# Kernel tuning notes

Hardware: AMD Instinct MI355X
Metric: run time of the kernel (lower is better)

## Reference

```python
import jax, jax.numpy as jnp
import numpy as np

VOL_RANGE = (-40.0, -40.0, -1.0, 40.0, 40.0, 5.4)
VOXEL = 0.8
SCENE = tuple(int((VOL_RANGE[i + 3] - VOL_RANGE[i]) / VOXEL) for i in range(3))  # (100, 100, 8)
B, G, F = 1, 128, 16


def _make_grid():
    # generate_grid(scene_shape, offset=0.5) * voxel_size + vol_range[:3]
    axes = [(jnp.arange(s, dtype=jnp.float32) + 0.5) * VOXEL + VOL_RANGE[i]
            for i, s in enumerate(SCENE)]
    gx, gy, gz = jnp.meshgrid(*axes, indexing='ij')
    return jnp.stack([gx, gy, gz], axis=-1).reshape(-1, 3)  # (N, 3)


def setup_inputs() -> dict:
    key = jax.random.key(0)
    k1, k2, k3, k4 = jax.random.split(key, 4)
    lo = jnp.array(VOL_RANGE[:3], dtype=jnp.float32)
    hi = jnp.array(VOL_RANGE[3:], dtype=jnp.float32)
    means3d = lo + jax.random.uniform(k1, (B, G, 3), dtype=jnp.float32) * (hi - lo)
    opacities = jax.random.uniform(k2, (B, G, 1), dtype=jnp.float32)
    features = jax.random.normal(k3, (B, G, F), dtype=jnp.float32)
    A = jax.random.normal(k4, (B, G, 3, 3), dtype=jnp.float32)
    covariances = jnp.einsum('bgij,bgkj->bgik', A, A) + 0.1 * jnp.eye(3, dtype=jnp.float32)
    return {
        'grid_coords': _make_grid(),
        'means3d': means3d,
        'opacities': opacities,
        'features': features,
        'covariances': covariances,
    }


def _splat_into_3d(grid_coords, means3d, opacities, covariances, features):
    # grid_coords: (N,3); means3d: (B,G,3); opacities: (B,G,1);
    # covariances: (B,G,3,3); features: (B,G,F)
    b, g, _ = means3d.shape
    n = grid_coords.shape[0]
    f = features.shape[-1]
    dtype = means3d.dtype

    def step(carry, xs):
        dens, feats, cnts = carry                 # (B,N,1), (B,N,F), (B,N,1)
        mean, opac, cov, feat = xs                # (B,3), (B,1), (B,3,3), (B,F)
        diff = grid_coords[None] - mean[:, None]  # (B,N,3)
        cov_inv = jnp.linalg.inv(cov)             # (B,3,3)
        maha = jnp.einsum('bni,bij,bnj->bn', diff, cov_inv, diff)[..., None]  # (B,N,1)
        mask = (maha <= 4.0).astype(dtype)        # (B,N,1)
        cnts = cnts + mask
        denom = jnp.maximum(cnts, 1e-6)
        w = jnp.exp(-0.5 * maha)                  # (B,N,1)
        d_g = opac[:, None] * w                   # (B,N,1)
        dens = dens + mask * (d_g - dens) / denom
        f_g = (opac * feat)[:, None] * w          # (B,N,F)
        feats = feats + mask * (f_g - feats) / denom
        return (dens, feats, cnts), None

    init = (jnp.zeros((b, n, 1), dtype),
            jnp.zeros((b, n, f), dtype),
            jnp.zeros((b, n, 1), dtype))
    xs = (jnp.swapaxes(means3d, 0, 1),
          jnp.swapaxes(opacities, 0, 1),
          jnp.swapaxes(covariances, 0, 1),
          jnp.swapaxes(features, 0, 1))
    (dens, feats, _), _ = jax.lax.scan(step, init, xs)
    return dens, feats


def reference(grid_coords, means3d, opacities, features, covariances):
    dens, feats = _splat_into_3d(grid_coords, means3d, opacities, covariances, features)
    b = dens.shape[0]
    dens = dens.reshape(b, *SCENE, 1)
    feats = feats.reshape(b, *SCENE, feats.shape[-1])
    return dens, feats
```

## Files before the change

### kernel.cpp

```cpp
#include <hip/hip_runtime.h>
#include <hip/hip_bf16.h>


#define GV_GMAX 128
#define GV_F 16

__global__ __launch_bounds__(256)
void GaussianVoxelizer_40467181863368_kernel(
    const float* __restrict__ grid,
    const float* __restrict__ means,
    const float* __restrict__ opac,
    const float* __restrict__ feats,
    const float* __restrict__ covs,
    float* __restrict__ out_dens,
    float* __restrict__ out_feat,
    int N, int G)
{
    __shared__ float s_mean[GV_GMAX][3];
    __shared__ float s_op[GV_GMAX];
    __shared__ float s_inv[GV_GMAX][6];
    __shared__ float s_feat[GV_GMAX][GV_F];

    const int t = threadIdx.x;

    for (int g = t; g < G; g += blockDim.x) {
        const float c00 = covs[g * 9 + 0];
        const float c01 = covs[g * 9 + 1];
        const float c02 = covs[g * 9 + 2];
        const float c11 = covs[g * 9 + 4];
        const float c12 = covs[g * 9 + 5];
        const float c22 = covs[g * 9 + 8];
        const float m00 = c11 * c22 - c12 * c12;
        const float m01 = c02 * c12 - c01 * c22;
        const float m02 = c01 * c12 - c02 * c11;
        const float det = c00 * m00 + c01 * m01 + c02 * m02;
        const float rdet = 1.0f / det;
        s_inv[g][0] = m00 * rdet;
        s_inv[g][1] = m01 * rdet;
        s_inv[g][2] = m02 * rdet;
        s_inv[g][3] = (c00 * c22 - c02 * c02) * rdet;
        s_inv[g][4] = (c01 * c02 - c00 * c12) * rdet;
        s_inv[g][5] = (c00 * c11 - c01 * c01) * rdet;

        s_mean[g][0] = means[g * 3 + 0];
        s_mean[g][1] = means[g * 3 + 1];
        s_mean[g][2] = means[g * 3 + 2];
        s_op[g] = opac[g];
        #pragma unroll
        for (int f = 0; f < GV_F; ++f) s_feat[g][f] = feats[g * GV_F + f];
    }
    __syncthreads();

    const int n = blockIdx.x * blockDim.x + t;
    if (n >= N) return;

    const float px = grid[n * 3 + 0];
    const float py = grid[n * 3 + 1];
    const float pz = grid[n * 3 + 2];

    float cnt = 0.0f;
    float sum_d = 0.0f;
    float sum_f[GV_F];
    #pragma unroll
    for (int f = 0; f < GV_F; ++f) sum_f[f] = 0.0f;

    for (int g = 0; g < G; ++g) {
        const float dx = px - s_mean[g][0];
        const float dy = py - s_mean[g][1];
        const float dz = pz - s_mean[g][2];
        const float maha =
            s_inv[g][0] * dx * dx + s_inv[g][3] * dy * dy + s_inv[g][5] * dz * dz +
            2.0f * (s_inv[g][1] * dx * dy + s_inv[g][2] * dx * dz + s_inv[g][4] * dy * dz);
        if (maha <= 4.0f) {
            const float w = __expf(-0.5f * maha) * s_op[g];
            cnt += 1.0f;
            sum_d += w;
            #pragma unroll
            for (int f = 0; f < GV_F; ++f) sum_f[f] += w * s_feat[g][f];
        }
    }

    const float inv_c = (cnt > 0.0f) ? (1.0f / cnt) : 0.0f;
    out_dens[n] = sum_d * inv_c;

    float4* fo = (float4*)(out_feat + (size_t)n * GV_F);
    #pragma unroll
    for (int q = 0; q < 4; ++q) {
        fo[q] = make_float4(sum_f[4 * q + 0] * inv_c,
                            sum_f[4 * q + 1] * inv_c,
                            sum_f[4 * q + 2] * inv_c,
                            sum_f[4 * q + 3] * inv_c);
    }
}

extern "C" void kernel_launch(void* const* d_in, const int* in_sizes, int n_in,
                              void* d_out, int out_size, void* d_ws, size_t ws_size,
                              hipStream_t stream) {
    const float* grid  = (const float*)d_in[0];
    const float* means = (const float*)d_in[1];
    const float* opac  = (const float*)d_in[2];
    const float* feats = (const float*)d_in[3];
    const float* covs  = (const float*)d_in[4];

    const int N = in_sizes[0] / 3;
    const int G = in_sizes[2];

    float* out_dens = (float*)d_out;
    float* out_feat = (float*)d_out + N;

    const int block = 256;
    const int grid_n = (N + block - 1) / block;
    GaussianVoxelizer_40467181863368_kernel<<<grid_n, block, 0, stream>>>(
        grid, means, opac, feats, covs, out_dens, out_feat, N, G);
}
```

Measured before the change: 77.16 us.

## Split Gaussian loop across waves with shared-memory reduction per voxel

Each 256-thread block now handles 64 voxels instead of 256. Its four wavefronts each process a quarter of the Gaussians for the same voxels, and the partial counts, densities and features are summed in shared memory before the final normalization and store. This launches about four times as many blocks and shortens each thread's serial loop. The aim is better occupancy and load balance across CUs than the previous few hundred blocks gave. The cost is that every block repeats the Gaussian parameter setup, plus an extra barrier and a roughly 18 KB shared reduction buffer.

```diff
diff --git a/kernel.cpp b/kernel.cpp
--- a/kernel.cpp
+++ b/kernel.cpp
@@ -4,6 +4,9 @@
 
 #define GV_GMAX 128
 #define GV_F 16
+#define GV_NV 64
+#define GV_NW 4
+#define GV_RW (GV_F + 2)
 
 __global__ __launch_bounds__(256)
 void GaussianVoxelizer_40467181863368_kernel(
@@ -20,6 +23,7 @@
     __shared__ float s_op[GV_GMAX];
     __shared__ float s_inv[GV_GMAX][6];
     __shared__ float s_feat[GV_GMAX][GV_F];
+    __shared__ float s_red[GV_NW][GV_NV][GV_RW];
 
     const int t = threadIdx.x;
 
@@ -51,12 +55,20 @@
     }
     __syncthreads();
 
-    const int n = blockIdx.x * blockDim.x + t;
-    if (n >= N) return;
+    const int wave = t >> 6;
+    const int lane = t & 63;
+    const int n = blockIdx.x * GV_NV + lane;
 
-    const float px = grid[n * 3 + 0];
-    const float py = grid[n * 3 + 1];
-    const float pz = grid[n * 3 + 2];
+    float px = 0.0f, py = 0.0f, pz = 0.0f;
+    if (n < N) {
+        px = grid[n * 3 + 0];
+        py = grid[n * 3 + 1];
+        pz = grid[n * 3 + 2];
+    }
+
+    const int chunk = (G + GV_NW - 1) / GV_NW;
+    const int g0 = wave * chunk;
+    const int g1 = (g0 + chunk < G) ? (g0 + chunk) : G;
 
     float cnt = 0.0f;
     float sum_d = 0.0f;
@@ -64,32 +76,60 @@
     #pragma unroll
     for (int f = 0; f < GV_F; ++f) sum_f[f] = 0.0f;
 
-    for (int g = 0; g < G; ++g) {
-        const float dx = px - s_mean[g][0];
-        const float dy = py - s_mean[g][1];
-        const float dz = pz - s_mean[g][2];
-        const float maha =
-            s_inv[g][0] * dx * dx + s_inv[g][3] * dy * dy + s_inv[g][5] * dz * dz +
-            2.0f * (s_inv[g][1] * dx * dy + s_inv[g][2] * dx * dz + s_inv[g][4] * dy * dz);
-        if (maha <= 4.0f) {
-            const float w = __expf(-0.5f * maha) * s_op[g];
-            cnt += 1.0f;
-            sum_d += w;
-            #pragma unroll
-            for (int f = 0; f < GV_F; ++f) sum_f[f] += w * s_feat[g][f];
+    if (n < N) {
+        #pragma unroll 4
+        for (int g = g0; g < g1; ++g) {
+            const float dx = px - s_mean[g][0];
+            const float dy = py - s_mean[g][1];
+            const float dz = pz - s_mean[g][2];
+            const float maha =
+                s_inv[g][0] * dx * dx + s_inv[g][3] * dy * dy + s_inv[g][5] * dz * dz +
+                2.0f * (s_inv[g][1] * dx * dy + s_inv[g][2] * dx * dz + s_inv[g][4] * dy * dz);
+            if (maha <= 4.0f) {
+                const float w = __expf(-0.5f * maha) * s_op[g];
+                cnt += 1.0f;
+                sum_d += w;
+                #pragma unroll
+                for (int f = 0; f < GV_F; ++f) sum_f[f] += w * s_feat[g][f];
+            }
         }
     }
 
-    const float inv_c = (cnt > 0.0f) ? (1.0f / cnt) : 0.0f;
-    out_dens[n] = sum_d * inv_c;
+    {
+        float* r = &s_red[wave][lane][0];
+        r[0] = cnt;
+        r[1] = sum_d;
+        #pragma unroll
+        for (int f = 0; f < GV_F; ++f) r[2 + f] = sum_f[f];
+    }
+    __syncthreads();
 
-    float4* fo = (float4*)(out_feat + (size_t)n * GV_F);
-    #pragma unroll
-    for (int q = 0; q < 4; ++q) {
-        fo[q] = make_float4(sum_f[4 * q + 0] * inv_c,
-                            sum_f[4 * q + 1] * inv_c,
-                            sum_f[4 * q + 2] * inv_c,
-                            sum_f[4 * q + 3] * inv_c);
+    if (t < GV_NV) {
+        const int n2 = blockIdx.x * GV_NV + t;
+        if (n2 < N) {
+            float c = 0.0f, d = 0.0f;
+            float ff[GV_F];
+            #pragma unroll
+            for (int f = 0; f < GV_F; ++f) ff[f] = 0.0f;
+            #pragma unroll
+            for (int w = 0; w < GV_NW; ++w) {
+                const float* r = &s_red[w][t][0];
+                c += r[0];
+                d += r[1];
+                #pragma unroll
+                for (int f = 0; f < GV_F; ++f) ff[f] += r[2 + f];
+            }
+            const float inv_c = (c > 0.0f) ? (1.0f / c) : 0.0f;
+            out_dens[n2] = d * inv_c;
+            float4* fo = (float4*)(out_feat + (size_t)n2 * GV_F);
+            #pragma unroll
+            for (int q = 0; q < 4; ++q) {
+                fo[q] = make_float4(ff[4 * q + 0] * inv_c,
+                                    ff[4 * q + 1] * inv_c,
+                                    ff[4 * q + 2] * inv_c,
+                                    ff[4 * q + 3] * inv_c);
+            }
+        }
     }
 }
 
@@ -109,7 +149,7 @@
     float* out_feat = (float*)d_out + N;
 
     const int block = 256;
-    const int grid_n = (N + block - 1) / block;
+    const int grid_n = (N + GV_NV - 1) / GV_NV;
     GaussianVoxelizer_40467181863368_kernel<<<grid_n, block, 0, stream>>>(
         grid, means, opac, feats, covs, out_dens, out_feat, N, G);
 }
```

Result: faster. 71.44 us (-7.4%).

## Switch voxelizer from per-voxel gather to per-Gaussian bounding-box scatter with atomics

Applied to the files above, without the earlier changes.

Instead of every voxel testing all Gaussians, each Gaussian gets its own block. That block visits only the voxels inside a 2-sigma axis-aligned box and adds density, feature and count contributions with atomicAdd. Voxel centres are computed from the fixed scene constants, so the grid buffer is no longer read. A zero-fill kernel and a final normalisation kernel are added around the scatter pass. This avoids evaluating Gaussians far from a voxel, at the cost of three launches, extra output traffic and atomic contention, and only 128 blocks in the main pass.

```diff
diff --git a/kernel.cpp b/kernel.cpp
--- a/kernel.cpp
+++ b/kernel.cpp
@@ -2,101 +2,140 @@
 #include <hip/hip_bf16.h>
 
 
-#define GV_GMAX 128
 #define GV_F 16
+#define GV_SX 100
+#define GV_SY 100
+#define GV_SZ 8
+#define GV_LOX (-40.0f)
+#define GV_LOY (-40.0f)
+#define GV_LOZ (-1.0f)
+#define GV_VOX 0.8f
 
 __global__ __launch_bounds__(256)
-void GaussianVoxelizer_40467181863368_kernel(
-    const float* __restrict__ grid,
-    const float* __restrict__ means,
-    const float* __restrict__ opac,
-    const float* __restrict__ feats,
-    const float* __restrict__ covs,
-    float* __restrict__ out_dens,
-    float* __restrict__ out_feat,
-    int N, int G)
+void gv_zero(float4* __restrict__ out4, int n_out4,
+             float4* __restrict__ cnt4, int n_cnt4)
 {
-    __shared__ float s_mean[GV_GMAX][3];
-    __shared__ float s_op[GV_GMAX];
-    __shared__ float s_inv[GV_GMAX][6];
-    __shared__ float s_feat[GV_GMAX][GV_F];
+    const int i = blockIdx.x * blockDim.x + threadIdx.x;
+    const int stride = gridDim.x * blockDim.x;
+    const float4 z = make_float4(0.f, 0.f, 0.f, 0.f);
+    for (int j = i; j < n_out4; j += stride) out4[j] = z;
+    for (int j = i; j < n_cnt4; j += stride) cnt4[j] = z;
+}
 
-    const int t = threadIdx.x;
+__global__ __launch_bounds__(256)
+void gv_accum(const float* __restrict__ means,
+              const float* __restrict__ opac,
+              const float* __restrict__ feats,
+              const float* __restrict__ covs,
+              float* __restrict__ cnt,
+              float* __restrict__ out_dens,
+              float* __restrict__ out_feat,
+              int G)
+{
+    const int g = blockIdx.x;
+    if (g >= G) return;
 
-    for (int g = t; g < G; g += blockDim.x) {
-        const float c00 = covs[g * 9 + 0];
-        const float c01 = covs[g * 9 + 1];
-        const float c02 = covs[g * 9 + 2];
-        const float c11 = covs[g * 9 + 4];
-        const float c12 = covs[g * 9 + 5];
-        const float c22 = covs[g * 9 + 8];
-        const float m00 = c11 * c22 - c12 * c12;
-        const float m01 = c02 * c12 - c01 * c22;
-        const float m02 = c01 * c12 - c02 * c11;
-        const float det = c00 * m00 + c01 * m01 + c02 * m02;
-        const float rdet = 1.0f / det;
-        s_inv[g][0] = m00 * rdet;
-        s_inv[g][1] = m01 * rdet;
-        s_inv[g][2] = m02 * rdet;
-        s_inv[g][3] = (c00 * c22 - c02 * c02) * rdet;
-        s_inv[g][4] = (c01 * c02 - c00 * c12) * rdet;
-        s_inv[g][5] = (c00 * c11 - c01 * c01) * rdet;
+    const float mx = means[g * 3 + 0];
+    const float my = means[g * 3 + 1];
+    const float mz = means[g * 3 + 2];
+    const float c00 = covs[g * 9 + 0];
+    const float c01 = covs[g * 9 + 1];
+    const float c02 = covs[g * 9 + 2];
+    const float c11 = covs[g * 9 + 4];
+    const float c12 = covs[g * 9 + 5];
+    const float c22 = covs[g * 9 + 8];
 
-        s_mean[g][0] = means[g * 3 + 0];
-        s_mean[g][1] = means[g * 3 + 1];
-        s_mean[g][2] = means[g * 3 + 2];
-        s_op[g] = opac[g];
-        #pragma unroll
-        for (int f = 0; f < GV_F; ++f) s_feat[g][f] = feats[g * GV_F + f];
-    }
-    __syncthreads();
+    const float rx = 2.0f * sqrtf(c00);
+    const float ry = 2.0f * sqrtf(c11);
+    const float rz = 2.0f * sqrtf(c22);
+    const int ix0 = max(0,         (int)floorf((mx - rx - GV_LOX) / GV_VOX - 0.5f));
+    const int ix1 = min(GV_SX - 1, (int)ceilf ((mx + rx - GV_LOX) / GV_VOX - 0.5f));
+    const int iy0 = max(0,         (int)floorf((my - ry - GV_LOY) / GV_VOX - 0.5f));
+    const int iy1 = min(GV_SY - 1, (int)ceilf ((my + ry - GV_LOY) / GV_VOX - 0.5f));
+    const int iz0 = max(0,         (int)floorf((mz - rz - GV_LOZ) / GV_VOX - 0.5f));
+    const int iz1 = min(GV_SZ - 1, (int)ceilf ((mz + rz - GV_LOZ) / GV_VOX - 0.5f));
+    if (ix0 > ix1 || iy0 > iy1 || iz0 > iz1) return;
 
-    const int n = blockIdx.x * blockDim.x + t;
-    if (n >= N) return;
+    const float m00 = c11 * c22 - c12 * c12;
+    const float m01 = c02 * c12 - c01 * c22;
+    const float m02 = c01 * c12 - c02 * c11;
+    const float det = c00 * m00 + c01 * m01 + c02 * m02;
+    const float s = -0.5f / det;
+    const float k00 = m00 * s;
+    const float k01 = m01 * (2.0f * s);
+    const float k02 = m02 * (2.0f * s);
+    const float k11 = (c00 * c22 - c02 * c02) * s;
+    const float k12 = (c01 * c02 - c00 * c12) * (2.0f * s);
+    const float k22 = (c00 * c11 - c01 * c01) * s;
 
-    const float px = grid[n * 3 + 0];
-    const float py = grid[n * 3 + 1];
-    const float pz = grid[n * 3 + 2];
+    const float op = opac[g];
+    float fo_w[GV_F];
+    #pragma unroll
+    for (int j = 0; j < GV_F; ++j) fo_w[j] = op * feats[g * GV_F + j];
 
-    float cnt = 0.0f;
-    float sum_d = 0.0f;
-    float sum_f[GV_F];
-    #pragma unroll
-    for (int f = 0; f < GV_F; ++f) sum_f[f] = 0.0f;
+    const int nx = ix1 - ix0 + 1;
+    const int ny = iy1 - iy0 + 1;
+    const int nz = iz1 - iz0 + 1;
+    const int nyz = ny * nz;
+    const int total = nx * nyz;
 
-    for (int g = 0; g < G; ++g) {
-        const float dx = px - s_mean[g][0];
-        const float dy = py - s_mean[g][1];
-        const float dz = pz - s_mean[g][2];
-        const float maha =
-            s_inv[g][0] * dx * dx + s_inv[g][3] * dy * dy + s_inv[g][5] * dz * dz +
-            2.0f * (s_inv[g][1] * dx * dy + s_inv[g][2] * dx * dz + s_inv[g][4] * dy * dz);
-        if (maha <= 4.0f) {
-            const float w = __expf(-0.5f * maha) * s_op[g];
-            cnt += 1.0f;
-            sum_d += w;
+    for (int idx = threadIdx.x; idx < total; idx += 256) {
+        int ix = idx / nyz;
+        int rem = idx - ix * nyz;
+        int iy = rem / nz;
+        int iz = rem - iy * nz;
+        ix += ix0; iy += iy0; iz += iz0;
+
+        const float cx = ((float)ix + 0.5f) * GV_VOX + GV_LOX;
+        const float cy = ((float)iy + 0.5f) * GV_VOX + GV_LOY;
+        const float cz = ((float)iz + 0.5f) * GV_VOX + GV_LOZ;
+        const float dx = cx - mx;
+        const float dy = cy - my;
+        const float dz = cz - mz;
+        float a = k00 * dx;
+        a = fmaf(k01, dy, a);
+        a = fmaf(k02, dz, a);
+        float tt = a * dx;
+        float b = k11 * dy;
+        b = fmaf(k12, dz, b);
+        tt = fmaf(b, dy, tt);
+        tt = fmaf(k22 * dz, dz, tt);
+
+        if (tt >= -2.0f) {
+            const float w = __expf(tt);
+            const int n = (ix * GV_SY + iy) * GV_SZ + iz;
+            atomicAdd(&cnt[n], 1.0f);
+            atomicAdd(&out_dens[n], op * w);
+            float* fp = out_feat + (size_t)n * GV_F;
             #pragma unroll
-            for (int f = 0; f < GV_F; ++f) sum_f[f] += w * s_feat[g][f];
+            for (int j = 0; j < GV_F; ++j) atomicAdd(&fp[j], fo_w[j] * w);
         }
     }
+}
 
-    const float inv_c = (cnt > 0.0f) ? (1.0f / cnt) : 0.0f;
-    out_dens[n] = sum_d * inv_c;
-
+__global__ __launch_bounds__(256)
+void gv_final(const float* __restrict__ cnt,
+              float* __restrict__ out_dens,
+              float* __restrict__ out_feat,
+              int N)
+{
+    const int n = blockIdx.x * blockDim.x + threadIdx.x;
+    if (n >= N) return;
+    const float c = cnt[n];
+    const float inv = (c > 0.0f) ? (1.0f / c) : 0.0f;
+    out_dens[n] *= inv;
     float4* fo = (float4*)(out_feat + (size_t)n * GV_F);
     #pragma unroll
     for (int q = 0; q < 4; ++q) {
-        fo[q] = make_float4(sum_f[4 * q + 0] * inv_c,
-                            sum_f[4 * q + 1] * inv_c,
-                            sum_f[4 * q + 2] * inv_c,
-                            sum_f[4 * q + 3] * inv_c);
+        float4 v = fo[q];
+        v.x *= inv; v.y *= inv; v.z *= inv; v.w *= inv;
+        fo[q] = v;
     }
 }
 
 extern "C" void kernel_launch(void* const* d_in, const int* in_sizes, int n_in,
                               void* d_out, int out_size, void* d_ws, size_t ws_size,
                               hipStream_t stream) {
-    const float* grid  = (const float*)d_in[0];
     const float* means = (const float*)d_in[1];
     const float* opac  = (const float*)d_in[2];
     const float* feats = (const float*)d_in[3];
@@ -105,11 +144,17 @@
     const int N = in_sizes[0] / 3;
     const int G = in_sizes[2];
 
+    float* cnt      = (float*)d_ws;
     float* out_dens = (float*)d_out;
     float* out_feat = (float*)d_out + N;
 
-    const int block = 256;
-    const int grid_n = (N + block - 1) / block;
-    GaussianVoxelizer_40467181863368_kernel<<<grid_n, block, 0, stream>>>(
-        grid, means, opac, feats, covs, out_dens, out_feat, N, G);
+    const int n_out4 = (N * (GV_F + 1)) / 4;
+    const int n_cnt4 = N / 4;
+    const int zgrid = (n_out4 + 255) / 256;
+    gv_zero<<<zgrid, 256, 0, stream>>>((float4*)d_out, n_out4, (float4*)cnt, n_cnt4);
+
+    gv_accum<<<G, 256, 0, stream>>>(means, opac, feats, covs,
+                                    cnt, out_dens, out_feat, G);
+
+    gv_final<<<(N + 255) / 256, 256, 0, stream>>>(cnt, out_dens, out_feat, N);
 }
```

New measurement: 85.10 us. +10.3%, slower.
